# Kernel optimization log

Measured on AMD Instinct MI355X. Metric: run time of the kernel, lower is better.

## Reference

```python
import jax, jax.numpy as jnp
import numpy as np

B, S, D, DM, H = 2, 2048, 1024, 1024, 16
DH = D // H
EPS = 1e-5


def layernorm(x, g, b):
    m = jnp.mean(x, axis=-1, keepdims=True)
    v = jnp.mean(jnp.square(x - m), axis=-1, keepdims=True)
    return (x - m) * jax.lax.rsqrt(v + EPS) * g + b


def setup_inputs() -> dict:
    key = jax.random.key(0)
    ks = jax.random.split(key, 16)
    std = 0.02
    p = {
        'x': jax.random.normal(ks[0], (B, S, D), jnp.float32),
        'h': jnp.zeros((B, DM), jnp.float32),
        'c': jnp.zeros((B, DM), jnp.float32),
        'Wq': jax.random.normal(ks[1], (D, D), jnp.float32) * std,
        'Wk': jax.random.normal(ks[2], (D, D), jnp.float32) * std,
        'Wv': jax.random.normal(ks[3], (D, D), jnp.float32) * std,
        'Wo': jax.random.normal(ks[4], (D, D), jnp.float32) * std,
        'Wmk': jax.random.normal(ks[5], (DM, D), jnp.float32) * std,
        'Wmv': jax.random.normal(ks[6], (DM, D), jnp.float32) * std,
        'Wih': jax.random.normal(ks[7], (D, 4 * DM), jnp.float32) * std,
        'Whh': jax.random.normal(ks[8], (DM, 4 * DM), jnp.float32) * std,
        'b_ih': jnp.zeros((4 * DM,), jnp.float32),
        'b_hh': jnp.zeros((4 * DM,), jnp.float32),
        'W1': jax.random.normal(ks[9], (D, 4 * D), jnp.float32) * std,
        'bf1': jnp.zeros((4 * D,), jnp.float32),
        'W2': jax.random.normal(ks[10], (4 * D, D), jnp.float32) * std,
        'bf2': jnp.zeros((D,), jnp.float32),
        'g1': jnp.ones((D,), jnp.float32), 'be1': jnp.zeros((D,), jnp.float32),
        'g2': jnp.ones((D,), jnp.float32), 'be2': jnp.zeros((D,), jnp.float32),
        'g3': jnp.ones((D,), jnp.float32), 'be3': jnp.zeros((D,), jnp.float32),
        'Wmp': jax.random.normal(ks[11], (DM, D), jnp.float32) * std,
    }
    return p


def reference(x, h, c, Wq, Wk, Wv, Wo, Wmk, Wmv, Wih, Whh, b_ih, b_hh,
              W1, bf1, W2, bf2, g1, be1, g2, be2, g3, be3, Wmp):
    xn = layernorm(x, g1, be1)
    # projections, split heads: [B,S,D] -> [B,H,S,DH]
    def heads(t):
        return t.reshape(B, -1, H, DH).transpose(0, 2, 1, 3)
    Q = heads(xn @ Wq)
    Ks = heads(xn @ Wk)
    Vs = heads(xn @ Wv)
    Km = (h @ Wmk).reshape(B, 1, H, DH).transpose(0, 2, 1, 3)  # [B,H,1,DH]
    Vm = (h @ Wmv).reshape(B, 1, H, DH).transpose(0, 2, 1, 3)
    K = jnp.concatenate([Km, Ks], axis=2)  # [B,H,S+1,DH]
    V = jnp.concatenate([Vm, Vs], axis=2)
    scores = jnp.einsum('bhqd,bhkd->bhqk', Q, K) / jnp.sqrt(jnp.float32(DH))
    attn = jax.nn.softmax(scores, axis=-1)
    ao = jnp.einsum('bhqk,bhkd->bhqd', attn, V)
    ao = ao.transpose(0, 2, 1, 3).reshape(B, S, D)
    attended = x + ao @ Wo
    # LSTM step on mean-pooled tokens (torch LSTMCell gate order: i,f,g,o)
    pooled = jnp.mean(attended, axis=1)  # [B,D]
    gates = pooled @ Wih + b_ih + h @ Whh + b_hh
    i, f, g, o = jnp.split(gates, 4, axis=-1)
    new_c = jax.nn.sigmoid(f) * c + jax.nn.sigmoid(i) * jnp.tanh(g)
    new_h = jax.nn.sigmoid(o) * jnp.tanh(new_c)
    mixed = attended + (new_h @ Wmp)[:, None, :]
    hn = layernorm(mixed, g2, be2)
    ffn = jax.nn.gelu(hn @ W1 + bf1, approximate=False) @ W2 + bf2
    out = layernorm(mixed + ffn, g3, be3)
    return (out, new_h, new_c)
```

## Files before the change

kernel.cpp:

```cpp
#include <hip/hip_runtime.h>
#include <hip/hip_bf16.h>
#include <math.h>

#define BB 2
#define SS 2048
#define DD 1024
#define HH 16
#define RR (BB*SS)
#define KSTRIDE 2064
#define MB (1024ull*1024ull)

typedef unsigned short u16;
typedef unsigned int u32;
typedef __attribute__((ext_vector_type(8))) short short8v;
typedef __attribute__((ext_vector_type(4))) float f32x4;
typedef __attribute__((ext_vector_type(16))) float f32x16;
typedef __attribute__((ext_vector_type(4))) u16 u16x4;

__device__ __forceinline__ u16 f2bf(float f){
    union { __hip_bfloat16 h; u16 u; } c; c.h = __float2bfloat16(f); return c.u;
}
__device__ __forceinline__ u32 pk2(float a, float b){
    return (u32)f2bf(a) | ((u32)f2bf(b) << 16);
}
__device__ __forceinline__ float exp2_raw(float x){
    float r;
    asm("v_exp_f32 %0, %1" : "=v"(r) : "v"(x));
    return r;
}
__device__ __forceinline__ float erf_fast(float x){
    float ax = fabsf(x);
    float t = __builtin_amdgcn_rcpf(1.0f + 0.3275911f*ax);
    float y = t*(0.254829592f + t*(-0.284496736f + t*(1.421413741f + t*(-1.453152027f + t*1.061405429f))));
    float r = 1.0f - y*__expf(-ax*ax);
    return copysignf(r, x);
}

#define GLL16(gp, lp) __builtin_amdgcn_global_load_lds( \
    (const __attribute__((address_space(1))) void*)(gp), \
    (__attribute__((address_space(3))) void*)(lp), 16, 0, 0)

__global__ __launch_bounds__(256) void ln_kernel(const float* __restrict__ in,
    const float* __restrict__ mproj, const float* __restrict__ g, const float* __restrict__ be,
    float* __restrict__ mixed_out, float* __restrict__ outf, u16* __restrict__ outb)
{
    int row = blockIdx.x; int b = row / SS; int tid = threadIdx.x;
    float4 v = ((const float4*)(in + (size_t)row*DD))[tid];
    if (mproj){
        float4 mp = ((const float4*)(mproj + (size_t)b*DD))[tid];
        v.x+=mp.x; v.y+=mp.y; v.z+=mp.z; v.w+=mp.w;
        ((float4*)(mixed_out + (size_t)row*DD))[tid] = v;
    }
    float s = v.x+v.y+v.z+v.w, s2 = v.x*v.x+v.y*v.y+v.z*v.z+v.w*v.w;
    #pragma unroll
    for (int off=32; off>0; off>>=1){ s += __shfl_down(s,off); s2 += __shfl_down(s2,off); }
    __shared__ float red[2][4];
    if ((tid&63)==0){ red[0][tid>>6]=s; red[1][tid>>6]=s2; }
    __syncthreads();
    float st = red[0][0]+red[0][1]+red[0][2]+red[0][3];
    float s2t= red[1][0]+red[1][1]+red[1][2]+red[1][3];
    float mean = st*(1.f/DD); float var = s2t*(1.f/DD)-mean*mean;
    float rs = rsqrtf(var + 1e-5f);
    float4 gg=((const float4*)g)[tid], bb2=((const float4*)be)[tid];
    float o0=(v.x-mean)*rs*gg.x+bb2.x, o1=(v.y-mean)*rs*gg.y+bb2.y;
    float o2=(v.z-mean)*rs*gg.z+bb2.z, o3=(v.w-mean)*rs*gg.w+bb2.w;
    if (outf){ float4 o={o0,o1,o2,o3}; ((float4*)(outf+(size_t)row*DD))[tid]=o; }
    if (outb){ u16x4 o={f2bf(o0),f2bf(o1),f2bf(o2),f2bf(o3)}; ((u16x4*)(outb+(size_t)row*DD))[tid]=o; }
}

__global__ __launch_bounds__(256) void ln3f_kernel(const float* __restrict__ p0,
    const float* __restrict__ p1a, const float* __restrict__ p1b,
    const float* __restrict__ bias, const float* __restrict__ resid,
    const float* __restrict__ g, const float* __restrict__ be, float* __restrict__ out)
{
    int row = blockIdx.x; int tid = threadIdx.x;
    const float* p1 = (row < 2048) ? (p1a + (size_t)row*DD) : (p1b + (size_t)(row-2048)*DD);
    float4 a  = ((const float4*)(p0 + (size_t)row*DD))[tid];
    float4 b  = ((const float4*)p1)[tid];
    float4 bi = ((const float4*)bias)[tid];
    float4 rs4= ((const float4*)(resid + (size_t)row*DD))[tid];
    float4 v = {a.x+b.x+bi.x+rs4.x, a.y+b.y+bi.y+rs4.y, a.z+b.z+bi.z+rs4.z, a.w+b.w+bi.w+rs4.w};
    float s = v.x+v.y+v.z+v.w, s2 = v.x*v.x+v.y*v.y+v.z*v.z+v.w*v.w;
    #pragma unroll
    for (int off=32; off>0; off>>=1){ s += __shfl_down(s,off); s2 += __shfl_down(s2,off); }
    __shared__ float red[2][4];
    if ((tid&63)==0){ red[0][tid>>6]=s; red[1][tid>>6]=s2; }
    __syncthreads();
    float st = red[0][0]+red[0][1]+red[0][2]+red[0][3];
    float s2t= red[1][0]+red[1][1]+red[1][2]+red[1][3];
    float mean = st*(1.f/DD); float var = s2t*(1.f/DD)-mean*mean;
    float rs = rsqrtf(var + 1e-5f);
    float4 gg=((const float4*)g)[tid], bb2=((const float4*)be)[tid];
    float4 o;
    o.x=(v.x-mean)*rs*gg.x+bb2.x; o.y=(v.y-mean)*rs*gg.y+bb2.y;
    o.z=(v.z-mean)*rs*gg.z+bb2.z; o.w=(v.w-mean)*rs*gg.w+bb2.w;
    ((float4*)(out + (size_t)row*DD))[tid] = o;
}

__global__ __launch_bounds__(256) void tr6_kernel(const float* __restrict__ Wq, const float* __restrict__ Wk,
    const float* __restrict__ Wv, const float* __restrict__ Wo,
    const float* __restrict__ W1, const float* __restrict__ W2,
    u16* __restrict__ WqkvT, u16* __restrict__ WoT, u16* __restrict__ W1T, u16* __restrict__ W2T)
{
    __shared__ float t[32][33];
    int bid = blockIdx.x;
    const float* in; u16* out; int K, N, n0, k0;
    if (bid < 3072){
        int m = bid >> 10, r = bid & 1023;
        in = (m==0) ? Wq : (m==1) ? Wk : Wv;
        out = WqkvT + (size_t)m*1024*1024;
        K = 1024; N = 1024; n0 = (r & 31)*32; k0 = (r >> 5)*32;
    } else if (bid < 4096){
        int r = bid - 3072;
        in = Wo; out = WoT; K = 1024; N = 1024; n0 = (r & 31)*32; k0 = (r >> 5)*32;
    } else if (bid < 8192){
        int r = bid - 4096;
        in = W1; out = W1T; K = 1024; N = 4096; n0 = (r & 127)*32; k0 = (r >> 7)*32;
    } else {
        int r = bid - 8192;
        in = W2; out = W2T; K = 4096; N = 1024; n0 = (r & 31)*32; k0 = (r >> 5)*32;
    }
    int tx = threadIdx.x & 31, ty = threadIdx.x >> 5;
    #pragma unroll
    for (int i=0;i<4;i++){ int k = ty + i*8; t[k][tx] = in[(size_t)(k0+k)*N + n0 + tx]; }
    __syncthreads();
    #pragma unroll
    for (int i=0;i<4;i++){ int n = ty + i*8; out[(size_t)(n0+n)*K + k0 + tx] = f2bf(t[tx][n]); }
}

#define MODE_QKV  0
#define MODE_F32R 3
#define MODE_GELU 4
#define MODE_PART 6

__global__ __launch_bounds__(256) void mgemm(const u16* __restrict__ A, const u16* __restrict__ BT,
    int nbx, int Kc, int kchunks, int mode,
    const float* __restrict__ bias, const float* __restrict__ resid, float scale,
    void* __restrict__ Cout, void* __restrict__ C2a, void* __restrict__ C2b)
{
    int tid=threadIdx.x, l=tid&63, w=tid>>6;
    int nwg = gridDim.x;
    int qq = nwg >> 3;
    int bid = blockIdx.x;
    int swz = (bid & 7)*qq + (bid >> 3);
    int tiles = nwg / kchunks;
    int chunk = swz / tiles;
    int t2 = swz % tiles;
    int sby = t2 / (nbx*8);
    int rem = t2 - sby*(nbx*8);
    int sbx = rem >> 6;
    int ci  = rem & 63;
    int bx = sbx*8 + (ci&7);
    int by = sby*8 + (ci>>3);

    int bm = by*128, bn = bx*128;
    int N = nbx*128;
    int lda = Kc*kchunks;
    int koff = chunk*Kc;
    int wr = w>>1, wc = w&1;
    f32x4 acc[4][4];
    #pragma unroll
    for(int i=0;i<4;i++)
        #pragma unroll
        for(int j=0;j<4;j++)
            #pragma unroll
            for(int r=0;r<4;r++) acc[i][j][r]=0.f;

    __shared__ __align__(16) u16 Al[2][4096];
    __shared__ __align__(16) u16 Bl[2][4096];
    int srow = (w<<4) + (l>>2);
    int sph  = l&3;
    const int NT = Kc >> 5;

    auto stage = [&](int buf, int kt){
        #pragma unroll
        for (int r=0;r<2;r++){
            int rowA = srow + r*64;
            int sl = sph ^ ((rowA>>1)&3);
            const u16* gA = A + (size_t)(bm+rowA)*lda + koff + kt*32 + sl*8;
            GLL16(gA, (char*)&Al[buf][0] + r*4096 + w*1024);
            const u16* gB = BT + (size_t)(bn+rowA)*lda + koff + kt*32 + sl*8;
            GLL16(gB, (char*)&Bl[buf][0] + r*4096 + w*1024);
        }
    };

    int cur=0;
    stage(0,0);
    __syncthreads();
    for (int kt=0; kt<NT; kt++){
        if (kt+1<NT) stage(cur^1, kt+1);
        short8v af[4], bf[4];
        #pragma unroll
        for (int mi=0;mi<4;mi++){
            int row = wr*64 + mi*16 + (l&15);
            int sl = (l>>4) ^ ((row>>1)&3);
            af[mi] = *(const short8v*)((const char*)&Al[cur][0] + row*64 + sl*16);
        }
        #pragma unroll
        for (int ni=0;ni<4;ni++){
            int row = wc*64 + ni*16 + (l&15);
            int sl = (l>>4) ^ ((row>>1)&3);
            bf[ni] = *(const short8v*)((const char*)&Bl[cur][0] + row*64 + sl*16);
        }
        #pragma unroll
        for (int mi=0;mi<4;mi++)
            #pragma unroll
            for (int ni=0;ni<4;ni++)
                acc[mi][ni] = __builtin_amdgcn_mfma_f32_16x16x32_bf16(bf[ni], af[mi], acc[mi][ni], 0,0,0);
        __syncthreads();
        cur ^= 1;
    }

    #pragma unroll
    for (int mi=0;mi<4;mi++){
        int m = bm + wr*64 + mi*16 + (l&15);
        #pragma unroll
        for (int ni=0;ni<4;ni++){
            int nb = bn + wc*64 + ni*16 + ((l>>4)<<2);
            f32x4 v = acc[mi][ni];
            if (mode==MODE_QKV){
                if (nb < 1024){
                    u16x4 o;
                    #pragma unroll
                    for (int r=0;r<4;r++) o[r] = f2bf(v[r]*scale);
                    *(u16x4*)((u16*)Cout + (size_t)m*1024 + nb) = o;
                } else if (nb < 2048){
                    int cc = nb-1024; int hh = cc>>6, dh = cc&63;
                    int b2 = m>>11, key = m&2047;
                    u16x4 o;
                    #pragma unroll
                    for (int r=0;r<4;r++) o[r] = f2bf(v[r]);
                    *(u16x4*)((u16*)C2a + ((size_t)(b2*HH+hh)*KSTRIDE + key)*64 + dh) = o;
                } else {
                    int cc = nb-2048; int hh = cc>>6, dh = cc&63;
                    int b2 = m>>11, key = m&2047;
                    #pragma unroll
                    for (int r=0;r<4;r++)
                        ((u16*)C2b)[((size_t)(b2*HH+hh)*64 + dh + r)*KSTRIDE + key] = f2bf(v[r]);
                }
            } else if (mode==MODE_F32R){
                float4 rs = *(const float4*)(resid + (size_t)m*N + nb);
                float4 o = {v[0]+rs.x, v[1]+rs.y, v[2]+rs.z, v[3]+rs.w};
                *(float4*)((float*)Cout + (size_t)m*N + nb) = o;
            } else if (mode==MODE_GELU){
                float4 bi = *(const float4*)(bias + nb);
                float t0=v[0]+bi.x, t1=v[1]+bi.y, t2=v[2]+bi.z, t3=v[3]+bi.w;
                u16x4 o;
                o[0]=f2bf(0.5f*t0*(1.0f+erf_fast(t0*0.70710678118654752f)));
                o[1]=f2bf(0.5f*t1*(1.0f+erf_fast(t1*0.70710678118654752f)));
                o[2]=f2bf(0.5f*t2*(1.0f+erf_fast(t2*0.70710678118654752f)));
                o[3]=f2bf(0.5f*t3*(1.0f+erf_fast(t3*0.70710678118654752f)));
                *(u16x4*)((u16*)Cout + (size_t)m*N + nb) = o;
            } else {
                float4 o = {v[0],v[1],v[2],v[3]};
                if (chunk==0)       *(float4*)((float*)Cout + (size_t)m*N + nb) = o;
                else if (m < 2048)  *(float4*)((float*)C2a  + (size_t)m*N + nb) = o;
                else                *(float4*)((float*)C2b  + (size_t)(m-2048)*N + nb) = o;
            }
        }
    }
}

__global__ __launch_bounds__(256) void attn_mfma(const u16* __restrict__ Qb, const u16* __restrict__ Kb,
    const u16* __restrict__ VTb, u16* __restrict__ ao)
{
    __shared__ __align__(16) u16 Kl[3][4096];
    __shared__ __align__(16) u16 Vl[3][4096];
    int tid=threadIdx.x, l=tid&63, w=tid>>6;
    int l31=l&31, hi=l>>5;
    int bid = blockIdx.x;
    int xcd = bid & 7, idx = bid >> 3;
    int bh = xcd*4 + (idx>>4);
    int qt = idx & 15;
    int b=bh>>4, h=bh&15;
    int qrow = qt*128 + w*32 + l31;

    const u16* qptr = Qb + (size_t)(b*SS + qrow)*DD + h*64;
    short8v qf[4];
    #pragma unroll
    for (int t=0;t<4;t++) qf[t] = *(const short8v*)(qptr + t*16 + hi*8);

    f32x16 so0, so1;
    #pragma unroll
    for (int i=0;i<16;i++){ so0[i]=0.f; so1[i]=0.f; }
    float l_run=0.f;

    int skey = (w<<3) + (l>>3);
    int ssl  = l&7;
    auto stage = [&](int buf, int kt){
        #pragma unroll
        for (int r=0;r<2;r++){
            int key = skey + r*32;
            int slot = ssl ^ (key&7);
            const u16* gK = Kb + ((size_t)bh*KSTRIDE + kt*64 + key)*64 + slot*8;
            GLL16(gK, (char*)&Kl[buf][0] + r*4096 + w*1024);
            const u16* gV = VTb + ((size_t)bh*64 + key)*KSTRIDE + kt*64 + slot*8;
            GLL16(gV, (char*)&Vl[buf][0] + r*4096 + w*1024);
        }
    };

    auto QK = [&](int bf, f32x16& s0, f32x16& s1){
        #pragma unroll
        for (int i=0;i<16;i++){ s0[i]=0.f; s1[i]=0.f; }
        __builtin_amdgcn_s_setprio(1);
        #pragma unroll
        for (int t=0;t<4;t++){
            int sl = (2*t+hi) ^ (l31&7);
            short8v kf0 = *(const short8v*)((const char*)&Kl[bf][0] + l31*128 + sl*16);
            s0 = __builtin_amdgcn_mfma_f32_32x32x16_bf16(kf0, qf[t], s0, 0,0,0);
            short8v kf1 = *(const short8v*)((const char*)&Kl[bf][0] + (32+l31)*128 + sl*16);
            s1 = __builtin_amdgcn_mfma_f32_32x32x16_bf16(kf1, qf[t], s1, 0,0,0);
        }
        __builtin_amdgcn_s_setprio(0);
    };

    auto SMPV = [&](int bf, f32x16& s0, f32x16& s1){
        float psum = 0.f;
        #pragma unroll
        for (int r=0;r<16;r++){
            float p=exp2_raw(s0[r]); s0[r]=p; psum+=p;
            float q=exp2_raw(s1[r]); s1[r]=q; psum+=q;
        }
        psum += __shfl_xor(psum, 32);
        l_run += psum;
        short8v pf[4];
        #pragma unroll
        for (int t=0;t<4;t++){
            u32 a0,a1,b0,b1;
            if (t==0){ a0=pk2(s0[0],s0[1]);   a1=pk2(s0[2],s0[3]);   b0=pk2(s0[4],s0[5]);   b1=pk2(s0[6],s0[7]); }
            else if (t==1){ a0=pk2(s0[8],s0[9]);   a1=pk2(s0[10],s0[11]); b0=pk2(s0[12],s0[13]); b1=pk2(s0[14],s0[15]); }
            else if (t==2){ a0=pk2(s1[0],s1[1]);   a1=pk2(s1[2],s1[3]);   b0=pk2(s1[4],s1[5]);   b1=pk2(s1[6],s1[7]); }
            else          { a0=pk2(s1[8],s1[9]);   a1=pk2(s1[10],s1[11]); b0=pk2(s1[12],s1[13]); b1=pk2(s1[14],s1[15]); }
            u32 sx0 = hi ? a0 : b0, sx1 = hi ? a1 : b1;
            u32 r0 = (u32)__shfl_xor((int)sx0, 32);
            u32 r1 = (u32)__shfl_xor((int)sx1, 32);
            union { u32 u[4]; short8v v; } cvt;
            cvt.u[0] = hi ? r0 : a0;
            cvt.u[1] = hi ? r1 : a1;
            cvt.u[2] = hi ? b0 : r0;
            cvt.u[3] = hi ? b1 : r1;
            pf[t] = cvt.v;
        }
        __builtin_amdgcn_s_setprio(1);
        #pragma unroll
        for (int t=0;t<4;t++){
            int sl = (2*t+hi) ^ (l31&7);
            short8v vf0 = *(const short8v*)((const char*)&Vl[bf][0] + l31*128 + sl*16);
            so0 = __builtin_amdgcn_mfma_f32_32x32x16_bf16(vf0, pf[t], so0, 0,0,0);
            short8v vf1 = *(const short8v*)((const char*)&Vl[bf][0] + (32+l31)*128 + sl*16);
            so1 = __builtin_amdgcn_mfma_f32_32x32x16_bf16(vf1, pf[t], so1, 0,0,0);
        }
        __builtin_amdgcn_s_setprio(0);
    };

    const int NTILE = 33;
    int bufA = 0, bufB = 1, bufC = 2;
    stage(0, 0);
    stage(1, 1);
    __syncthreads();

    f32x16 sA0, sA1, sB0, sB1;
    QK(bufA, sA0, sA1);

    auto ITER = [&](f32x16& c0, f32x16& c1, f32x16& n0, f32x16& n1, int t){
        if (t+2 < NTILE) stage(bufC, t+2);
        QK(bufB, n0, n1);
        SMPV(bufA, c0, c1);
        __syncthreads();
        int tmp = bufA; bufA = bufB; bufB = bufC; bufC = tmp;
    };
    #pragma unroll 1
    for (int tt=0; tt<16; tt++){
        ITER(sA0, sA1, sB0, sB1, 2*tt);
        ITER(sB0, sB1, sA0, sA1, 2*tt+1);
    }
    #pragma unroll
    for (int r=0;r<16;r++){
        int k0 = 2048 + (r&3) + 8*(r>>2) + 4*hi;
        if (k0 >= 2049) sA0[r] = -1e30f;
        sA1[r] = -1e30f;
    }
    SMPV(bufA, sA0, sA1);

    float inv = 1.f / l_run;
    u16* aop = ao + (size_t)(b*SS + qrow)*DD + h*64;
    #pragma unroll
    for (int rg=0; rg<4; rg++){
        int dh0 = rg*8 + 4*hi;
        u16x4 o0, o1;
        #pragma unroll
        for (int j=0;j<4;j++){ o0[j]=f2bf(so0[rg*4+j]*inv); o1[j]=f2bf(so1[rg*4+j]*inv); }
        *(u16x4*)(aop + dh0) = o0;
        *(u16x4*)(aop + 32 + dh0) = o1;
    }
}

__global__ __launch_bounds__(256) void vecmat_part(const float* __restrict__ vec,
    const float* __restrict__ W, float* __restrict__ part, int K, int N)
{
    int b = blockIdx.z, kc = blockIdx.y;
    int j = blockIdx.x*256 + threadIdx.x;
    int k0 = kc * (K >> 3);
    float acc = 0.0f;
    #pragma unroll 4
    for (int k = k0; k < k0 + (K >> 3); k++)
        acc += vec[(size_t)b*K + k] * W[(size_t)k*N + j];
    part[((size_t)b*8 + kc)*N + j] = acc;
}

__global__ __launch_bounds__(256) void vecmat_red(const float* __restrict__ part,
    float* __restrict__ out, int N)
{
    int b = blockIdx.y;
    int j = blockIdx.x*256 + threadIdx.x;
    float acc = 0.0f;
    #pragma unroll
    for (int kc = 0; kc < 8; kc++) acc += part[((size_t)b*8 + kc)*N + j];
    out[(size_t)b*N + j] = acc;
}

__global__ __launch_bounds__(256) void vecmat2_part(const float* __restrict__ vec,
    const float* __restrict__ Wa, const float* __restrict__ Wb, float* __restrict__ part)
{
    int b = blockIdx.z, kc = blockIdx.y;
    int j = blockIdx.x*256 + threadIdx.x;
    int k0 = kc * 128;
    float accA = 0.0f, accB = 0.0f;
    #pragma unroll 4
    for (int k = k0; k < k0 + 128; k++){
        float v = vec[(size_t)b*DD + k];
        accA += v * Wa[(size_t)k*DD + j];
        accB += v * Wb[(size_t)k*DD + j];
    }
    part[((size_t)b*8 + kc)*2048 + j] = accA;
    part[((size_t)b*8 + kc)*2048 + 1024 + j] = accB;
}

__global__ __launch_bounds__(256) void vecmat2_red(const float* __restrict__ part,
    float* __restrict__ outA, float* __restrict__ outB)
{
    int b = blockIdx.y;
    int j = blockIdx.x*256 + threadIdx.x;
    float accA = 0.0f, accB = 0.0f;
    #pragma unroll
    for (int kc = 0; kc < 8; kc++){
        accA += part[((size_t)b*8 + kc)*2048 + j];
        accB += part[((size_t)b*8 + kc)*2048 + 1024 + j];
    }
    outA[(size_t)b*DD + j] = accA;
    outB[(size_t)b*DD + j] = accB;
}

__global__ __launch_bounds__(256) void fixup_kernel(const float* __restrict__ Kmb,
    const float* __restrict__ Vmb, u16* __restrict__ Kb, u16* __restrict__ VTb)
{
    int idx = blockIdx.x*256 + threadIdx.x;
    int b = idx>>10, j = idx&1023; int h=j>>6, dh=j&63; int bh=b*HH+h;
    Kb[((size_t)bh*KSTRIDE + 2048)*64 + dh] = f2bf(Kmb[idx]);
    VTb[((size_t)bh*64 + dh)*KSTRIDE + 2048] = f2bf(Vmb[idx]);
}

__global__ __launch_bounds__(256) void pool1_kernel(const float* __restrict__ att, float* __restrict__ ppart)
{
    int b = blockIdx.y, sc = blockIdx.x;
    int tid = threadIdx.x;
    float4 acc = {0,0,0,0};
    for (int s = 0; s < 32; s++) {
        int row = b*SS + sc*32 + s;
        float4 v = ((const float4*)(att + (size_t)row*DD))[tid];
        acc.x += v.x; acc.y += v.y; acc.z += v.z; acc.w += v.w;
    }
    ((float4*)(ppart + ((size_t)b*64 + sc)*DD))[tid] = acc;
}

__global__ __launch_bounds__(256) void pool2_kernel(const float* __restrict__ ppart, float* __restrict__ pooled)
{
    int b = blockIdx.y;
    int j = blockIdx.x*256 + threadIdx.x;
    float acc = 0.0f;
    for (int sc = 0; sc < 64; sc++) acc += ppart[((size_t)b*64 + sc)*DD + j];
    pooled[(size_t)b*DD + j] = acc * (1.0f/SS);
}

__global__ __launch_bounds__(256) void gates_part(const float* __restrict__ pooled,
    const float* __restrict__ h, const float* __restrict__ Wih, const float* __restrict__ Whh,
    float* __restrict__ part)
{
    int b = blockIdx.z, kc = blockIdx.y;
    int j = blockIdx.x*256 + threadIdx.x;
    int k0 = kc * 64;
    float acc = 0.0f;
    #pragma unroll 4
    for (int k = k0; k < k0 + 64; k++)
        acc += pooled[(size_t)b*DD + k] * Wih[(size_t)k*4*DD + j]
             + h[(size_t)b*DD + k]      * Whh[(size_t)k*4*DD + j];
    part[((size_t)b*16 + kc)*4*DD + j] = acc;
}

__device__ __forceinline__ float sigmoidf_(float x) { return 1.0f / (1.0f + __expf(-x)); }

__global__ __launch_bounds__(256) void lstm_kernel(const float* __restrict__ gpart,
    const float* __restrict__ b_ih, const float* __restrict__ b_hh,
    const float* __restrict__ c, float* __restrict__ newh_ws, float* __restrict__ out_tail)
{
    int idx = blockIdx.x*256 + threadIdx.x;
    int b = idx >> 10, d = idx & 1023;
    float sI = b_ih[d]          + b_hh[d];
    float sF = b_ih[DD + d]     + b_hh[DD + d];
    float sG = b_ih[2*DD + d]   + b_hh[2*DD + d];
    float sO = b_ih[3*DD + d]   + b_hh[3*DD + d];
    #pragma unroll
    for (int kc = 0; kc < 16; kc++){
        const float* gp = gpart + ((size_t)b*16 + kc)*4*DD;
        sI += gp[d]; sF += gp[DD + d]; sG += gp[2*DD + d]; sO += gp[3*DD + d];
    }
    float ig = sigmoidf_(sI);
    float fg = sigmoidf_(sF);
    float gg = tanhf(sG);
    float og = sigmoidf_(sO);
    float nc = fg * c[idx] + ig * gg;
    float nh = og * tanhf(nc);
    newh_ws[idx] = nh;
    out_tail[idx] = nh;
    out_tail[BB*DD + idx] = nc;
}

extern "C" void kernel_launch(void* const* d_in, const int* in_sizes, int n_in,
                              void* d_out, int out_size, void* d_ws, size_t ws_size,
                              hipStream_t stream) {
    const float* x    = (const float*)d_in[0];
    const float* h    = (const float*)d_in[1];
    const float* c    = (const float*)d_in[2];
    const float* Wq   = (const float*)d_in[3];
    const float* Wk   = (const float*)d_in[4];
    const float* Wv   = (const float*)d_in[5];
    const float* Wo   = (const float*)d_in[6];
    const float* Wmk  = (const float*)d_in[7];
    const float* Wmv  = (const float*)d_in[8];
    const float* Wih  = (const float*)d_in[9];
    const float* Whh  = (const float*)d_in[10];
    const float* b_ih = (const float*)d_in[11];
    const float* b_hh = (const float*)d_in[12];
    const float* W1   = (const float*)d_in[13];
    const float* bf1  = (const float*)d_in[14];
    const float* W2   = (const float*)d_in[15];
    const float* bf2  = (const float*)d_in[16];
    const float* g1   = (const float*)d_in[17];
    const float* be1  = (const float*)d_in[18];
    const float* g2   = (const float*)d_in[19];
    const float* be2  = (const float*)d_in[20];
    const float* g3   = (const float*)d_in[21];
    const float* be3  = (const float*)d_in[22];
    const float* Wmp  = (const float*)d_in[23];

    float* out = (float*)d_out;
    char* wsb  = (char*)d_ws;

    u16*   xn   = (u16*)(wsb + 0);
    u16*   hn   = (u16*)(wsb + 8*MB);
    float* p0   = (float*)(wsb + 0);
    u16*   Qbuf = (u16*)(wsb + 16*MB);
    u16*   Kbuf = (u16*)(wsb + 24*MB);
    u16*   VTb  = (u16*)(wsb + 33*MB);
    u16*   act  = (u16*)(wsb + 16*MB);
    u16*   ao   = (u16*)(wsb + 48*MB);
    float* p1a  = (float*)(wsb + 48*MB);
    float* attb = (float*)(wsb + 56*MB);
    u16*   WqkvT= (u16*)(wsb + 72*MB);
    u16*   WoT  = (u16*)(wsb + 78*MB);
    u16*   W1T  = (u16*)(wsb + 80*MB);
    float* p1b  = (float*)(wsb + 80*MB);
    u16*   W2T  = (u16*)(wsb + 88*MB);
    float* sm   = (float*)(wsb + 96*MB);
    float* Kmb     = sm;
    float* Vmb     = Kmb + 2048;
    float* pooled  = Vmb + 2048;
    float* newh    = pooled + 2048;
    float* mproj   = newh + 2048;
    float* vpart   = mproj + 2048;
    float* v2part  = vpart + 16384;
    float* gpart   = v2part + 32768;
    float* ppart   = gpart + 131072;

    tr6_kernel<<<12288, 256, 0, stream>>>(Wq, Wk, Wv, Wo, W1, W2, WqkvT, WoT, W1T, W2T);

    ln_kernel<<<RR, 256, 0, stream>>>(x, nullptr, g1, be1, nullptr, nullptr, xn);
    vecmat2_part<<<dim3(4,8,BB), 256, 0, stream>>>(h, Wmk, Wmv, v2part);
    vecmat2_red<<<dim3(4,BB), 256, 0, stream>>>(v2part, Kmb, Vmb);
    mgemm<<<24*32, 256, 0, stream>>>(xn, WqkvT, 24, 1024, 1, MODE_QKV, nullptr, nullptr,
                                     0.125f*1.44269504088896f, Qbuf, Kbuf, VTb);
    fixup_kernel<<<8, 256, 0, stream>>>(Kmb, Vmb, Kbuf, VTb);
    attn_mfma<<<512, 256, 0, stream>>>(Qbuf, Kbuf, VTb, ao);
    mgemm<<<8*32, 256, 0, stream>>>(ao, WoT, 8, 1024, 1, MODE_F32R, nullptr, x, 1.f, attb, nullptr, nullptr);
    pool1_kernel<<<dim3(64,BB), 256, 0, stream>>>(attb, ppart);
    pool2_kernel<<<dim3(4,BB), 256, 0, stream>>>(ppart, pooled);
    gates_part<<<dim3(16,16,BB), 256, 0, stream>>>(pooled, h, Wih, Whh, gpart);
    lstm_kernel<<<8, 256, 0, stream>>>(gpart, b_ih, b_hh, c, newh, out + (size_t)RR*DD);
    vecmat_part<<<dim3(4,8,BB), 256, 0, stream>>>(newh, Wmp, vpart, DD, DD);
    vecmat_red<<<dim3(4,BB), 256, 0, stream>>>(vpart, mproj, DD);
    ln_kernel<<<RR, 256, 0, stream>>>(attb, mproj, g2, be2, attb, nullptr, hn);
    mgemm<<<32*32, 256, 0, stream>>>(hn, W1T, 32, 1024, 1, MODE_GELU, bf1, nullptr, 1.f, act, nullptr, nullptr);
    mgemm<<<8*32*2, 256, 0, stream>>>(act, W2T, 8, 2048, 2, MODE_PART, nullptr, nullptr, 1.f, p0, p1a, p1b);
    ln3f_kernel<<<RR, 256, 0, stream>>>(p0, p1a, p1b, bf2, attb, g3, be3, out);
}
```

Before: 329.7 us.

## Add 256x256-tile 8-wave GEMM with fine-grained LDS pipelining for QKV and FFN1

```diff
diff --git a/kernel.cpp b/kernel.cpp
--- a/kernel.cpp
+++ b/kernel.cpp
@@ -39,6 +39,12 @@
 #define GLL16(gp, lp) __builtin_amdgcn_global_load_lds( \
     (const __attribute__((address_space(1))) void*)(gp), \
     (__attribute__((address_space(3))) void*)(lp), 16, 0, 0)
+
+#define VMCNT8 asm volatile("s_waitcnt vmcnt(8)" ::: "memory")
+#define VMCNT4 asm volatile("s_waitcnt vmcnt(4)" ::: "memory")
+#define VMCNT0 asm volatile("s_waitcnt vmcnt(0)" ::: "memory")
+#define SBAR   __builtin_amdgcn_s_barrier()
+#define SCHEDB __builtin_amdgcn_sched_barrier(0)
 
 __global__ __launch_bounds__(256) void ln_kernel(const float* __restrict__ in,
     const float* __restrict__ mproj, const float* __restrict__ g, const float* __restrict__ be,
@@ -128,97 +134,168 @@
     for (int i=0;i<4;i++){ int n = ty + i*8; out[(size_t)(n0+n)*K + k0 + tx] = f2bf(t[tx][n]); }
 }
 
-#define MODE_QKV  0
-#define MODE_F32R 3
-#define MODE_GELU 4
-#define MODE_PART 6
-
-__global__ __launch_bounds__(256) void mgemm(const u16* __restrict__ A, const u16* __restrict__ BT,
-    int nbx, int Kc, int kchunks, int mode,
-    const float* __restrict__ bias, const float* __restrict__ resid, float scale,
+__global__ __launch_bounds__(512) void mgemm256(const u16* __restrict__ A, const u16* __restrict__ BT,
+    int nbx, int K, int mode, const float* __restrict__ bias, float scale,
     void* __restrict__ Cout, void* __restrict__ C2a, void* __restrict__ C2b)
 {
-    int tid=threadIdx.x, l=tid&63, w=tid>>6;
-    int nwg = gridDim.x;
-    int qq = nwg >> 3;
+    __shared__ __align__(16) u16 lds[2][2][2][256*32];
+    int tid = threadIdx.x, l = tid&63, w = tid>>6;
+    int wr = w>>2, wc = w&3;
+    int nwg = gridDim.x, q8 = nwg>>3;
     int bid = blockIdx.x;
-    int swz = (bid & 7)*qq + (bid >> 3);
-    int tiles = nwg / kchunks;
-    int chunk = swz / tiles;
-    int t2 = swz % tiles;
-    int sby = t2 / (nbx*8);
-    int rem = t2 - sby*(nbx*8);
-    int sbx = rem >> 6;
-    int ci  = rem & 63;
-    int bx = sbx*8 + (ci&7);
-    int by = sby*8 + (ci>>3);
-
-    int bm = by*128, bn = bx*128;
-    int N = nbx*128;
-    int lda = Kc*kchunks;
-    int koff = chunk*Kc;
-    int wr = w>>1, wc = w&1;
-    f32x4 acc[4][4];
-    #pragma unroll
-    for(int i=0;i<4;i++)
-        #pragma unroll
-        for(int j=0;j<4;j++)
+    int swz = (bid & 7)*q8 + (bid >> 3);
+    int by = swz / nbx, bx = swz % nbx;
+    int bm = by*256, bn = bx*256;
+    const int NT = K >> 6;
+
+    f32x4 acc[8][4];
+    #pragma unroll
+    for (int i=0;i<8;i++)
+        #pragma unroll
+        for (int j=0;j<4;j++)
             #pragma unroll
-            for(int r=0;r<4;r++) acc[i][j][r]=0.f;
-
-    __shared__ __align__(16) u16 Al[2][4096];
-    __shared__ __align__(16) u16 Bl[2][4096];
-    int srow = (w<<4) + (l>>2);
-    int sph  = l&3;
-    const int NT = Kc >> 5;
-
-    auto stage = [&](int buf, int kt){
-        #pragma unroll
-        for (int r=0;r<2;r++){
-            int rowA = srow + r*64;
-            int sl = sph ^ ((rowA>>1)&3);
-            const u16* gA = A + (size_t)(bm+rowA)*lda + koff + kt*32 + sl*8;
-            GLL16(gA, (char*)&Al[buf][0] + r*4096 + w*1024);
-            const u16* gB = BT + (size_t)(bn+rowA)*lda + koff + kt*32 + sl*8;
-            GLL16(gB, (char*)&Bl[buf][0] + r*4096 + w*1024);
+            for (int r=0;r<4;r++) acc[i][j][r]=0.f;
+
+    auto stage_plane = [&](int buf, int op, int ks, int tt){
+        const u16* base = op ? BT : A;
+        int tile0 = op ? bn : bm;
+        #pragma unroll
+        for (int i=0;i<2;i++){
+            int rbase = (w*2+i)*16;
+            int row = rbase + (l>>2);
+            int slotlog = (l&3) ^ ((row>>1)&3);
+            const u16* g = base + (size_t)(tile0 + row)*K + tt*64 + ks*32 + slotlog*8;
+            GLL16(g, (u16*)&lds[buf][op][ks][0] + rbase*32);
         }
     };
-
-    int cur=0;
-    stage(0,0);
-    __syncthreads();
-    for (int kt=0; kt<NT; kt++){
-        if (kt+1<NT) stage(cur^1, kt+1);
-        short8v af[4], bf[4];
-        #pragma unroll
-        for (int mi=0;mi<4;mi++){
-            int row = wr*64 + mi*16 + (l&15);
-            int sl = (l>>4) ^ ((row>>1)&3);
-            af[mi] = *(const short8v*)((const char*)&Al[cur][0] + row*64 + sl*16);
-        }
-        #pragma unroll
-        for (int ni=0;ni<4;ni++){
-            int row = wc*64 + ni*16 + (l&15);
-            int sl = (l>>4) ^ ((row>>1)&3);
-            bf[ni] = *(const short8v*)((const char*)&Bl[cur][0] + row*64 + sl*16);
-        }
-        #pragma unroll
-        for (int mi=0;mi<4;mi++)
-            #pragma unroll
-            for (int ni=0;ni<4;ni++)
-                acc[mi][ni] = __builtin_amdgcn_mfma_f32_16x16x32_bf16(bf[ni], af[mi], acc[mi][ni], 0,0,0);
-        __syncthreads();
-        cur ^= 1;
-    }
-
-    #pragma unroll
-    for (int mi=0;mi<4;mi++){
-        int m = bm + wr*64 + mi*16 + (l&15);
-        #pragma unroll
-        for (int ni=0;ni<4;ni++){
-            int nb = bn + wc*64 + ni*16 + ((l>>4)<<2);
-            f32x4 v = acc[mi][ni];
-            if (mode==MODE_QKV){
+    auto ds_a = [&](int buf, int ks, int ai) -> short8v {
+        int row = wr*128 + ai*16 + (l&15);
+        int slot = (l>>4) ^ ((row>>1)&3);
+        return *(const short8v*)((const char*)&lds[buf][0][ks][0] + row*64 + slot*16);
+    };
+    auto ds_b = [&](int buf, int ks, int bi) -> short8v {
+        int row = wc*64 + bi*16 + (l&15);
+        int slot = (l>>4) ^ ((row>>1)&3);
+        return *(const short8v*)((const char*)&lds[buf][1][ks][0] + row*64 + slot*16);
+    };
+
+    stage_plane(0,0,0,0); stage_plane(0,1,0,0);
+    stage_plane(0,0,1,0); stage_plane(0,1,1,0);
+    stage_plane(1,0,0,1); stage_plane(1,1,0,1);
+    VMCNT8;
+    SBAR; SCHEDB;
+
+    for (int t=0; t<NT; t++){
+        int buf = t&1, obuf = buf^1;
+        bool s1 = (t+1 < NT), s2 = (t+2 < NT);
+        short8v b0,b1,b2,b3, a0,a1,a2,a3;
+        b0=ds_b(buf,0,0); b1=ds_b(buf,0,1); b2=ds_b(buf,0,2); b3=ds_b(buf,0,3);
+        a0=ds_a(buf,0,0); a1=ds_a(buf,0,1); a2=ds_a(buf,0,2); a3=ds_a(buf,0,3);
+        if (s1) stage_plane(obuf,0,1,t+1);
+        __builtin_amdgcn_s_setprio(1);
+        acc[0][0]=__builtin_amdgcn_mfma_f32_16x16x32_bf16(b0,a0,acc[0][0],0,0,0);
+        acc[0][1]=__builtin_amdgcn_mfma_f32_16x16x32_bf16(b1,a0,acc[0][1],0,0,0);
+        acc[0][2]=__builtin_amdgcn_mfma_f32_16x16x32_bf16(b2,a0,acc[0][2],0,0,0);
+        acc[0][3]=__builtin_amdgcn_mfma_f32_16x16x32_bf16(b3,a0,acc[0][3],0,0,0);
+        acc[1][0]=__builtin_amdgcn_mfma_f32_16x16x32_bf16(b0,a1,acc[1][0],0,0,0);
+        acc[1][1]=__builtin_amdgcn_mfma_f32_16x16x32_bf16(b1,a1,acc[1][1],0,0,0);
+        acc[1][2]=__builtin_amdgcn_mfma_f32_16x16x32_bf16(b2,a1,acc[1][2],0,0,0);
+        acc[1][3]=__builtin_amdgcn_mfma_f32_16x16x32_bf16(b3,a1,acc[1][3],0,0,0);
+        acc[2][0]=__builtin_amdgcn_mfma_f32_16x16x32_bf16(b0,a2,acc[2][0],0,0,0);
+        acc[2][1]=__builtin_amdgcn_mfma_f32_16x16x32_bf16(b1,a2,acc[2][1],0,0,0);
+        acc[2][2]=__builtin_amdgcn_mfma_f32_16x16x32_bf16(b2,a2,acc[2][2],0,0,0);
+        acc[2][3]=__builtin_amdgcn_mfma_f32_16x16x32_bf16(b3,a2,acc[2][3],0,0,0);
+        acc[3][0]=__builtin_amdgcn_mfma_f32_16x16x32_bf16(b0,a3,acc[3][0],0,0,0);
+        acc[3][1]=__builtin_amdgcn_mfma_f32_16x16x32_bf16(b1,a3,acc[3][1],0,0,0);
+        acc[3][2]=__builtin_amdgcn_mfma_f32_16x16x32_bf16(b2,a3,acc[3][2],0,0,0);
+        acc[3][3]=__builtin_amdgcn_mfma_f32_16x16x32_bf16(b3,a3,acc[3][3],0,0,0);
+        __builtin_amdgcn_s_setprio(0);
+        SBAR; SCHEDB;
+        a0=ds_a(buf,0,4); a1=ds_a(buf,0,5); a2=ds_a(buf,0,6); a3=ds_a(buf,0,7);
+        if (s1) stage_plane(obuf,1,1,t+1);
+        __builtin_amdgcn_s_setprio(1);
+        acc[4][0]=__builtin_amdgcn_mfma_f32_16x16x32_bf16(b0,a0,acc[4][0],0,0,0);
+        acc[4][1]=__builtin_amdgcn_mfma_f32_16x16x32_bf16(b1,a0,acc[4][1],0,0,0);
+        acc[4][2]=__builtin_amdgcn_mfma_f32_16x16x32_bf16(b2,a0,acc[4][2],0,0,0);
+        acc[4][3]=__builtin_amdgcn_mfma_f32_16x16x32_bf16(b3,a0,acc[4][3],0,0,0);
+        acc[5][0]=__builtin_amdgcn_mfma_f32_16x16x32_bf16(b0,a1,acc[5][0],0,0,0);
+        acc[5][1]=__builtin_amdgcn_mfma_f32_16x16x32_bf16(b1,a1,acc[5][1],0,0,0);
+        acc[5][2]=__builtin_amdgcn_mfma_f32_16x16x32_bf16(b2,a1,acc[5][2],0,0,0);
+        acc[5][3]=__builtin_amdgcn_mfma_f32_16x16x32_bf16(b3,a1,acc[5][3],0,0,0);
+        acc[6][0]=__builtin_amdgcn_mfma_f32_16x16x32_bf16(b0,a2,acc[6][0],0,0,0);
+        acc[6][1]=__builtin_amdgcn_mfma_f32_16x16x32_bf16(b1,a2,acc[6][1],0,0,0);
+        acc[6][2]=__builtin_amdgcn_mfma_f32_16x16x32_bf16(b2,a2,acc[6][2],0,0,0);
+        acc[6][3]=__builtin_amdgcn_mfma_f32_16x16x32_bf16(b3,a2,acc[6][3],0,0,0);
+        acc[7][0]=__builtin_amdgcn_mfma_f32_16x16x32_bf16(b0,a3,acc[7][0],0,0,0);
+        acc[7][1]=__builtin_amdgcn_mfma_f32_16x16x32_bf16(b1,a3,acc[7][1],0,0,0);
+        acc[7][2]=__builtin_amdgcn_mfma_f32_16x16x32_bf16(b2,a3,acc[7][2],0,0,0);
+        acc[7][3]=__builtin_amdgcn_mfma_f32_16x16x32_bf16(b3,a3,acc[7][3],0,0,0);
+        __builtin_amdgcn_s_setprio(0);
+        if (s1) { VMCNT8; } else { VMCNT0; }
+        SBAR; SCHEDB;
+        b0=ds_b(buf,1,0); b1=ds_b(buf,1,1); b2=ds_b(buf,1,2); b3=ds_b(buf,1,3);
+        a0=ds_a(buf,1,0); a1=ds_a(buf,1,1); a2=ds_a(buf,1,2); a3=ds_a(buf,1,3);
+        if (s2) stage_plane(buf,0,0,t+2);
+        __builtin_amdgcn_s_setprio(1);
+        acc[0][0]=__builtin_amdgcn_mfma_f32_16x16x32_bf16(b0,a0,acc[0][0],0,0,0);
+        acc[0][1]=__builtin_amdgcn_mfma_f32_16x16x32_bf16(b1,a0,acc[0][1],0,0,0);
+        acc[0][2]=__builtin_amdgcn_mfma_f32_16x16x32_bf16(b2,a0,acc[0][2],0,0,0);
+        acc[0][3]=__builtin_amdgcn_mfma_f32_16x16x32_bf16(b3,a0,acc[0][3],0,0,0);
+        acc[1][0]=__builtin_amdgcn_mfma_f32_16x16x32_bf16(b0,a1,acc[1][0],0,0,0);
+        acc[1][1]=__builtin_amdgcn_mfma_f32_16x16x32_bf16(b1,a1,acc[1][1],0,0,0);
+        acc[1][2]=__builtin_amdgcn_mfma_f32_16x16x32_bf16(b2,a1,acc[1][2],0,0,0);
+        acc[1][3]=__builtin_amdgcn_mfma_f32_16x16x32_bf16(b3,a1,acc[1][3],0,0,0);
+        acc[2][0]=__builtin_amdgcn_mfma_f32_16x16x32_bf16(b0,a2,acc[2][0],0,0,0);
+        acc[2][1]=__builtin_amdgcn_mfma_f32_16x16x32_bf16(b1,a2,acc[2][1],0,0,0);
+        acc[2][2]=__builtin_amdgcn_mfma_f32_16x16x32_bf16(b2,a2,acc[2][2],0,0,0);
+        acc[2][3]=__builtin_amdgcn_mfma_f32_16x16x32_bf16(b3,a2,acc[2][3],0,0,0);
+        acc[3][0]=__builtin_amdgcn_mfma_f32_16x16x32_bf16(b0,a3,acc[3][0],0,0,0);
+        acc[3][1]=__builtin_amdgcn_mfma_f32_16x16x32_bf16(b1,a3,acc[3][1],0,0,0);
+        acc[3][2]=__builtin_amdgcn_mfma_f32_16x16x32_bf16(b2,a3,acc[3][2],0,0,0);
+        acc[3][3]=__builtin_amdgcn_mfma_f32_16x16x32_bf16(b3,a3,acc[3][3],0,0,0);
+        __builtin_amdgcn_s_setprio(0);
+        SBAR; SCHEDB;
+        a0=ds_a(buf,1,4); a1=ds_a(buf,1,5); a2=ds_a(buf,1,6); a3=ds_a(buf,1,7);
+        if (s2) stage_plane(buf,1,0,t+2);
+        __builtin_amdgcn_s_setprio(1);
+        acc[4][0]=__builtin_amdgcn_mfma_f32_16x16x32_bf16(b0,a0,acc[4][0],0,0,0);
+        acc[4][1]=__builtin_amdgcn_mfma_f32_16x16x32_bf16(b1,a0,acc[4][1],0,0,0);
+        acc[4][2]=__builtin_amdgcn_mfma_f32_16x16x32_bf16(b2,a0,acc[4][2],0,0,0);
+        acc[4][3]=__builtin_amdgcn_mfma_f32_16x16x32_bf16(b3,a0,acc[4][3],0,0,0);
+        acc[5][0]=__builtin_amdgcn_mfma_f32_16x16x32_bf16(b0,a1,acc[5][0],0,0,0);
+        acc[5][1]=__builtin_amdgcn_mfma_f32_16x16x32_bf16(b1,a1,acc[5][1],0,0,0);
+        acc[5][2]=__builtin_amdgcn_mfma_f32_16x16x32_bf16(b2,a1,acc[5][2],0,0,0);
+        acc[5][3]=__builtin_amdgcn_mfma_f32_16x16x32_bf16(b3,a1,acc[5][3],0,0,0);
+        acc[6][0]=__builtin_amdgcn_mfma_f32_16x16x32_bf16(b0,a2,acc[6][0],0,0,0);
+        acc[6][1]=__builtin_amdgcn_mfma_f32_16x16x32_bf16(b1,a2,acc[6][1],0,0,0);
+        acc[6][2]=__builtin_amdgcn_mfma_f32_16x16x32_bf16(b2,a2,acc[6][2],0,0,0);
+        acc[6][3]=__builtin_amdgcn_mfma_f32_16x16x32_bf16(b3,a2,acc[6][3],0,0,0);
+        acc[7][0]=__builtin_amdgcn_mfma_f32_16x16x32_bf16(b0,a3,acc[7][0],0,0,0);
+        acc[7][1]=__builtin_amdgcn_mfma_f32_16x16x32_bf16(b1,a3,acc[7][1],0,0,0);
+        acc[7][2]=__builtin_amdgcn_mfma_f32_16x16x32_bf16(b2,a3,acc[7][2],0,0,0);
+        acc[7][3]=__builtin_amdgcn_mfma_f32_16x16x32_bf16(b3,a3,acc[7][3],0,0,0);
+        __builtin_amdgcn_s_setprio(0);
+        if (s2) { VMCNT8; } else if (s1) { VMCNT4; } else { VMCNT0; }
+        SBAR; SCHEDB;
+    }
+
+    #pragma unroll
+    for (int ai=0; ai<8; ai++){
+        int m = bm + wr*128 + ai*16 + (l&15);
+        #pragma unroll
+        for (int bi=0; bi<4; bi++){
+            int nb = bn + wc*64 + bi*16 + ((l>>4)<<2);
+            f32x4 v = acc[ai][bi];
+            if (mode == 0){
+                float4 bv = *(const float4*)(bias + nb);
+                float t0=v[0]+bv.x, t1=v[1]+bv.y, t2=v[2]+bv.z, t3=v[3]+bv.w;
+                u16x4 o;
+                o[0]=f2bf(0.5f*t0*(1.0f+erf_fast(t0*0.70710678118654752f)));
+                o[1]=f2bf(0.5f*t1*(1.0f+erf_fast(t1*0.70710678118654752f)));
+                o[2]=f2bf(0.5f*t2*(1.0f+erf_fast(t2*0.70710678118654752f)));
+                o[3]=f2bf(0.5f*t3*(1.0f+erf_fast(t3*0.70710678118654752f)));
+                *(u16x4*)((u16*)Cout + (size_t)m*(nbx*256) + nb) = o;
+            } else {
                 if (nb < 1024){
                     u16x4 o;
                     #pragma unroll
@@ -238,19 +315,103 @@
                     for (int r=0;r<4;r++)
                         ((u16*)C2b)[((size_t)(b2*HH+hh)*64 + dh + r)*KSTRIDE + key] = f2bf(v[r]);
                 }
-            } else if (mode==MODE_F32R){
+            }
+        }
+    }
+}
+
+#define MODE_F32R 3
+#define MODE_PART 6
+
+__global__ __launch_bounds__(256) void mgemm(const u16* __restrict__ A, const u16* __restrict__ BT,
+    int nbx, int Kc, int kchunks, int mode,
+    const float* __restrict__ bias, const float* __restrict__ resid, float scale,
+    void* __restrict__ Cout, void* __restrict__ C2a, void* __restrict__ C2b)
+{
+    int tid=threadIdx.x, l=tid&63, w=tid>>6;
+    int nwg = gridDim.x;
+    int qq = nwg >> 3;
+    int bid = blockIdx.x;
+    int swz = (bid & 7)*qq + (bid >> 3);
+    int tiles = nwg / kchunks;
+    int chunk = swz / tiles;
+    int t2 = swz % tiles;
+    int sby = t2 / (nbx*8);
+    int rem = t2 - sby*(nbx*8);
+    int sbx = rem >> 6;
+    int ci  = rem & 63;
+    int bx = sbx*8 + (ci&7);
+    int by = sby*8 + (ci>>3);
+
+    int bm = by*128, bn = bx*128;
+    int N = nbx*128;
+    int lda = Kc*kchunks;
+    int koff = chunk*Kc;
+    int wr = w>>1, wc = w&1;
+    f32x4 acc[4][4];
+    #pragma unroll
+    for(int i=0;i<4;i++)
+        #pragma unroll
+        for(int j=0;j<4;j++)
+            #pragma unroll
+            for(int r=0;r<4;r++) acc[i][j][r]=0.f;
+
+    __shared__ __align__(16) u16 Al[2][4096];
+    __shared__ __align__(16) u16 Bl[2][4096];
+    int srow = (w<<4) + (l>>2);
+    int sph  = l&3;
+    const int NT = Kc >> 5;
+
+    auto stage = [&](int buf, int kt){
+        #pragma unroll
+        for (int r=0;r<2;r++){
+            int rowA = srow + r*64;
+            int sl = sph ^ ((rowA>>1)&3);
+            const u16* gA = A + (size_t)(bm+rowA)*lda + koff + kt*32 + sl*8;
+            GLL16(gA, (char*)&Al[buf][0] + r*4096 + w*1024);
+            const u16* gB = BT + (size_t)(bn+rowA)*lda + koff + kt*32 + sl*8;
+            GLL16(gB, (char*)&Bl[buf][0] + r*4096 + w*1024);
+        }
+    };
+
+    int cur=0;
+    stage(0,0);
+    __syncthreads();
+    for (int kt=0; kt<NT; kt++){
+        if (kt+1<NT) stage(cur^1, kt+1);
+        short8v af[4], bf[4];
+        #pragma unroll
+        for (int mi=0;mi<4;mi++){
+            int row = wr*64 + mi*16 + (l&15);
+            int sl = (l>>4) ^ ((row>>1)&3);
+            af[mi] = *(const short8v*)((const char*)&Al[cur][0] + row*64 + sl*16);
+        }
+        #pragma unroll
+        for (int ni=0;ni<4;ni++){
+            int row = wc*64 + ni*16 + (l&15);
+            int sl = (l>>4) ^ ((row>>1)&3);
+            bf[ni] = *(const short8v*)((const char*)&Bl[cur][0] + row*64 + sl*16);
+        }
+        #pragma unroll
+        for (int mi=0;mi<4;mi++)
+            #pragma unroll
+            for (int ni=0;ni<4;ni++)
+                acc[mi][ni] = __builtin_amdgcn_mfma_f32_16x16x32_bf16(bf[ni], af[mi], acc[mi][ni], 0,0,0);
+        __syncthreads();
+        cur ^= 1;
+    }
+
+    #pragma unroll
+    for (int mi=0;mi<4;mi++){
+        int m = bm + wr*64 + mi*16 + (l&15);
+        #pragma unroll
+        for (int ni=0;ni<4;ni++){
+            int nb = bn + wc*64 + ni*16 + ((l>>4)<<2);
+            f32x4 v = acc[mi][ni];
+            if (mode==MODE_F32R){
                 float4 rs = *(const float4*)(resid + (size_t)m*N + nb);
                 float4 o = {v[0]+rs.x, v[1]+rs.y, v[2]+rs.z, v[3]+rs.w};
                 *(float4*)((float*)Cout + (size_t)m*N + nb) = o;
-            } else if (mode==MODE_GELU){
-                float4 bi = *(const float4*)(bias + nb);
-                float t0=v[0]+bi.x, t1=v[1]+bi.y, t2=v[2]+bi.z, t3=v[3]+bi.w;
-                u16x4 o;
-                o[0]=f2bf(0.5f*t0*(1.0f+erf_fast(t0*0.70710678118654752f)));
-                o[1]=f2bf(0.5f*t1*(1.0f+erf_fast(t1*0.70710678118654752f)));
-                o[2]=f2bf(0.5f*t2*(1.0f+erf_fast(t2*0.70710678118654752f)));
-                o[3]=f2bf(0.5f*t3*(1.0f+erf_fast(t3*0.70710678118654752f)));
-                *(u16x4*)((u16*)Cout + (size_t)m*N + nb) = o;
             } else {
                 float4 o = {v[0],v[1],v[2],v[3]};
                 if (chunk==0)       *(float4*)((float*)Cout + (size_t)m*N + nb) = o;
@@ -587,8 +748,8 @@
     ln_kernel<<<RR, 256, 0, stream>>>(x, nullptr, g1, be1, nullptr, nullptr, xn);
     vecmat2_part<<<dim3(4,8,BB), 256, 0, stream>>>(h, Wmk, Wmv, v2part);
     vecmat2_red<<<dim3(4,BB), 256, 0, stream>>>(v2part, Kmb, Vmb);
-    mgemm<<<24*32, 256, 0, stream>>>(xn, WqkvT, 24, 1024, 1, MODE_QKV, nullptr, nullptr,
-                                     0.125f*1.44269504088896f, Qbuf, Kbuf, VTb);
+    mgemm256<<<192, 512, 0, stream>>>(xn, WqkvT, 12, 1024, 1, nullptr,
+                                      0.125f*1.44269504088896f, Qbuf, Kbuf, VTb);
     fixup_kernel<<<8, 256, 0, stream>>>(Kmb, Vmb, Kbuf, VTb);
     attn_mfma<<<512, 256, 0, stream>>>(Qbuf, Kbuf, VTb, ao);
     mgemm<<<8*32, 256, 0, stream>>>(ao, WoT, 8, 1024, 1, MODE_F32R, nullptr, x, 1.f, attb, nullptr, nullptr);
@@ -599,7 +760,7 @@
     vecmat_part<<<dim3(4,8,BB), 256, 0, stream>>>(newh, Wmp, vpart, DD, DD);
     vecmat_red<<<dim3(4,BB), 256, 0, stream>>>(vpart, mproj, DD);
     ln_kernel<<<RR, 256, 0, stream>>>(attb, mproj, g2, be2, attb, nullptr, hn);
-    mgemm<<<32*32, 256, 0, stream>>>(hn, W1T, 32, 1024, 1, MODE_GELU, bf1, nullptr, 1.f, act, nullptr, nullptr);
+    mgemm256<<<256, 512, 0, stream>>>(hn, W1T, 16, 1024, 0, bf1, 1.f, act, nullptr, nullptr);
     mgemm<<<8*32*2, 256, 0, stream>>>(act, W2T, 8, 2048, 2, MODE_PART, nullptr, nullptr, 1.f, p0, p1a, p1b);
     ln3f_kernel<<<RR, 256, 0, stream>>>(p0, p1a, p1b, bf2, attb, g3, be3, out);
 }
```

Result: faster. 303.9 us (-7.8%).
